# Kernel tuning notes

Measured on AMD Instinct MI355X. Metric: run time of the kernel, lower is better.

Reference implementation:

```python
import jax, jax.numpy as jnp
import numpy as np

B, T, D, U = 32, 1024, 2048, 1024

def setup_inputs() -> dict:
    key = jax.random.key(0)
    ks = jax.random.split(key, 8)
    s_d = 1.0 / np.sqrt(D)
    s_u = 1.0 / np.sqrt(U)
    return {
        "query": jax.random.normal(ks[0], (B, D), dtype=jnp.float32),
        "values": jax.random.normal(ks[1], (B, T, D), dtype=jnp.float32),
        "W1": jax.random.normal(ks[2], (D, U), dtype=jnp.float32) * s_d,
        "b1": jnp.zeros((U,), dtype=jnp.float32),
        "W2": jax.random.normal(ks[3], (D, U), dtype=jnp.float32) * s_d,
        "b2": jnp.zeros((U,), dtype=jnp.float32),
        "V": jax.random.normal(ks[4], (U, 1), dtype=jnp.float32) * s_u,
        "bv": jnp.zeros((1,), dtype=jnp.float32),
    }

def reference(query, values, W1, b1, W2, b2, V, bv):
    # keys: (B, T, U); query proj broadcast over time axis
    keys_proj = jnp.einsum('btd,du->btu', values, W1) + b1
    query_proj = (query @ W2 + b2)[:, None, :]          # (B, 1, U)
    score = jnp.tanh(keys_proj + query_proj) @ V + bv   # (B, T, 1)
    attention_weights = jax.nn.softmax(score, axis=1)   # (B, T, 1)
    context_vector = jnp.sum(attention_weights * values, axis=1)  # (B, D)
    return (context_vector, attention_weights)
```

## Files before the change

kernel.cpp:

```cpp
#include <hip/hip_runtime.h>
#include <math.h>

#define BB 32
#define TS 1024
#define DD 2048
#define UU 1024

typedef _Float16 f16x8 __attribute__((ext_vector_type(8)));
typedef _Float16 f16x2 __attribute__((ext_vector_type(2)));
typedef __fp16 fp16x2 __attribute__((ext_vector_type(2)));
typedef float f32x4 __attribute__((ext_vector_type(4)));

union H8 { f16x8 v; f16x2 p[4]; };

static __device__ inline f16x2 pk(float a, float b) {
  fp16x2 r = __builtin_amdgcn_cvt_pkrtz(a, b);
  return __builtin_bit_cast(f16x2, r);
}

static __device__ inline float fast_tanh(float x) {
  float e = __builtin_amdgcn_exp2f(x * 2.885390081777927f);
  return 1.f - 2.f * __builtin_amdgcn_rcpf(1.f + e);
}

static __device__ inline void gld16(const _Float16* g, _Float16* l) {
  __builtin_amdgcn_global_load_lds(
      (const __attribute__((address_space(1))) void*)g,
      (__attribute__((address_space(3))) void*)l, 16, 0, 0);
}

__global__ void zero_kernel(float* __restrict__ p) {
  p[blockIdx.x * 1024 + threadIdx.x] = 0.f;
}

__global__ __launch_bounds__(256) void qproj_kernel(
    const float* __restrict__ query, const float* __restrict__ W2,
    const float* __restrict__ b1, const float* __restrict__ b2,
    float* __restrict__ qpb) {
  __shared__ float qs[32][256];
  const int u0 = (blockIdx.x & 7) * 128;
  const int dsl = blockIdx.x >> 3;
  const int d0 = dsl * 256;
  const int tid = threadIdx.x;
  const int ul = tid & 127, half = tid >> 7;

  for (int i = tid; i < 32 * 64; i += 256) {
    int b = i >> 6, dq = i & 63;
    *(float4*)&qs[b][dq * 4] = *(const float4*)(query + b * DD + d0 + dq * 4);
  }
  __syncthreads();

  float acc[32];
#pragma unroll
  for (int b = 0; b < 32; ++b) acc[b] = 0.f;

  const float* wcol = W2 + (size_t)(d0 + half * 128) * UU + u0 + ul;
  for (int dd = 0; dd < 128; dd += 4) {
    float w0 = wcol[(size_t)(dd + 0) * UU];
    float w1 = wcol[(size_t)(dd + 1) * UU];
    float w2 = wcol[(size_t)(dd + 2) * UU];
    float w3 = wcol[(size_t)(dd + 3) * UU];
#pragma unroll
    for (int b = 0; b < 32; ++b) {
      float4 q4 = *(const float4*)&qs[b][half * 128 + dd];
      acc[b] += q4.x * w0 + q4.y * w1 + q4.z * w2 + q4.w * w3;
    }
  }

  const int u = u0 + ul;
  const float bias = (dsl == 0 && half == 0) ? (b1[u] + b2[u]) : 0.f;
#pragma unroll
  for (int b = 0; b < 32; ++b) atomicAdd(&qpb[b * UU + u], acc[b] + bias);
}

__global__ __launch_bounds__(256) void pack_values_kernel(
    const float* __restrict__ v, _Float16* __restrict__ vhp) {
  __shared__ _Float16 img[8192];
  const int mTile = blockIdx.x >> 5;
  const int kc = blockIdx.x & 31;
  const int tid = threadIdx.x;

#pragma unroll
  for (int i = 0; i < 4; ++i) {
    int idx = i * 256 + tid;
    int row = idx >> 3, khi = idx & 7;
    const float* src = v + ((size_t)(mTile * 128 + row)) * DD + kc * 64 + khi * 8;
    float4 x = *(const float4*)src;
    float4 y = *(const float4*)(src + 4);
    H8 h;
    h.p[0] = pk(x.x, x.y); h.p[1] = pk(x.z, x.w);
    h.p[2] = pk(y.x, y.y); h.p[3] = pk(y.z, y.w);
    *(f16x8*)&img[(khi * 128 + (row ^ khi)) * 8] = h.v;
  }
  __syncthreads();

  _Float16* out = vhp + ((size_t)mTile * 32 + kc) * 8192;
#pragma unroll
  for (int i = 0; i < 4; ++i) {
    int p = i * 256 + tid;
    int khi = p >> 7, row = p & 127;
    *(f16x8*)(out + (size_t)p * 8) = *(const f16x8*)&img[(khi * 128 + (row ^ khi)) * 8];
  }
}

__global__ __launch_bounds__(256) void pack_w1_kernel(
    const float* __restrict__ W1, _Float16* __restrict__ w1p) {
  __shared__ _Float16 img[8192];
  const int nTile = blockIdx.x >> 5;
  const int kc = blockIdx.x & 31;
  const int tid = threadIdx.x;

#pragma unroll
  for (int i = 0; i < 32; ++i) {
    int idx = i * 256 + tid;
    int ul = idx & 127, kl = idx >> 7;
    float x = W1[(size_t)(kc * 64 + kl) * UU + nTile * 128 + ul];
    int khi = kl >> 3, klo = kl & 7;
    img[(khi * 128 + (ul ^ khi)) * 8 + klo] = (_Float16)x;
  }
  __syncthreads();

  _Float16* out = w1p + ((size_t)nTile * 32 + kc) * 8192;
#pragma unroll
  for (int i = 0; i < 4; ++i) {
    int p = i * 256 + tid;
    int khi = p >> 7, row = p & 127;
    *(f16x8*)(out + (size_t)p * 8) = *(const f16x8*)&img[(khi * 128 + (row ^ khi)) * 8];
  }
}

__global__ __launch_bounds__(256) void score_gemm_p_kernel(
    const _Float16* __restrict__ vhp, const _Float16* __restrict__ w1p,
    const float* __restrict__ qpb, const float* __restrict__ V,
    float* __restrict__ score) {
  __shared__ _Float16 aS[8192];
  __shared__ _Float16 bS[8192];

  const int tid = threadIdx.x;
  const int r = blockIdx.x & 7, q = blockIdx.x >> 3;
  const int mTile = r * 32 + (q >> 3);
  const int nTile = q & 7;
  const int mBase = mTile * 128, nBase = nTile * 128;

  const int lane = tid & 63, wave = tid >> 6;
  const int wm = (wave & 1) * 64, wn = (wave >> 1) * 64;
  const int quad = lane >> 4, c16 = lane & 15;

  const _Float16* gA = vhp + (size_t)mTile * 32 * 8192 + lane * 8;
  const _Float16* gB = w1p + (size_t)nTile * 32 * 8192 + lane * 8;

  f32x4 acc[4][4];
#pragma unroll
  for (int mi = 0; mi < 4; ++mi)
#pragma unroll
    for (int ni = 0; ni < 4; ++ni) acc[mi][ni] = (f32x4)0.f;

  for (int kc = 0; kc < 32; ++kc) {
    __syncthreads();
#pragma unroll
    for (int j = 0; j < 4; ++j) {
      int s = wave * 4 + j;
      gld16(gA + (size_t)kc * 8192 + s * 512, &aS[s * 512]);
      gld16(gB + (size_t)kc * 8192 + s * 512, &bS[s * 512]);
    }
    __syncthreads();

#pragma unroll
    for (int h = 0; h < 2; ++h) {
      f16x8 af[4], bf[4];
#pragma unroll
      for (int i = 0; i < 4; ++i) {
        af[i] = *(const f16x8*)&aS[((h * 4 + quad) * 128 + wm + i * 16 + c16) * 8];
        bf[i] = *(const f16x8*)&bS[((h * 4 + quad) * 128 + wn + i * 16 + c16) * 8];
      }
#pragma unroll
      for (int mi = 0; mi < 4; ++mi)
#pragma unroll
        for (int ni = 0; ni < 4; ++ni)
          acc[mi][ni] = __builtin_amdgcn_mfma_f32_16x16x32_f16(
              af[mi], bf[ni], acc[mi][ni], 0, 0, 0);
    }
  }

  const int b = mBase >> 10;
  float qv[4], vv[4];
#pragma unroll
  for (int ni = 0; ni < 4; ++ni) {
    int ug = nBase + wn + ni * 16 + c16;
    qv[ni] = qpb[b * UU + ug];
    vv[ni] = V[ug];
  }
#pragma unroll
  for (int mi = 0; mi < 4; ++mi) {
#pragma unroll
    for (int reg = 0; reg < 4; ++reg) {
      float p = fast_tanh(acc[mi][0][reg] + qv[0]) * vv[0] +
                fast_tanh(acc[mi][1][reg] + qv[1]) * vv[1] +
                fast_tanh(acc[mi][2][reg] + qv[2]) * vv[2] +
                fast_tanh(acc[mi][3][reg] + qv[3]) * vv[3];
      p += __shfl_xor(p, 1, 64);
      p += __shfl_xor(p, 2, 64);
      p += __shfl_xor(p, 4, 64);
      p += __shfl_xor(p, 8, 64);
      if (c16 == 0) {
        int mrow = mBase + wm + mi * 16 + quad * 4 + reg;
        atomicAdd(&score[mrow], p);
      }
    }
  }
}

__global__ __launch_bounds__(256) void score_gemm_kernel(
    const float* __restrict__ values, const float* __restrict__ W1,
    const float* __restrict__ qpb, const float* __restrict__ V,
    float* __restrict__ score) {
  __shared__ _Float16 aS[4 * 128 * 8];
  __shared__ _Float16 bS[4 * 128 * 8];

  const int tid = threadIdx.x;
  const int mBase = (blockIdx.x >> 3) * 128;
  const int nBase = (blockIdx.x & 7) * 128;

  const int am = tid >> 1;
  const int akh = (tid & 1) * 16;
  const float* aG = values + (size_t)(mBase + am) * DD + akh;
  const int aOff0 = (((tid & 1) * 2) * 128 + am) * 8;
  const int bu2 = (tid & 63) * 2;
  const int bkq = tid >> 6;
  const float* bG = W1 + (size_t)(bkq * 8) * UU + nBase + bu2;
  const int bOff0 = (bkq * 128 + bu2) * 8;

  const int lane = tid & 63;
  const int wave = tid >> 6;
  const int wm = (wave & 1) * 64;
  const int wn = (wave >> 1) * 64;
  const int quad = lane >> 4;
  const int c16 = lane & 15;

  f32x4 acc[4][4];
#pragma unroll
  for (int mi = 0; mi < 4; ++mi)
#pragma unroll
    for (int ni = 0; ni < 4; ++ni) acc[mi][ni] = (f32x4)0.f;

  for (int k0 = 0; k0 < DD; k0 += 32) {
    float4 a0 = *(const float4*)(aG + k0 + 0);
    float4 a1 = *(const float4*)(aG + k0 + 4);
    float4 a2 = *(const float4*)(aG + k0 + 8);
    float4 a3 = *(const float4*)(aG + k0 + 12);
    const float* bRow = bG + (size_t)k0 * UU;
    float2 g0 = *(const float2*)(bRow + 0 * UU);
    float2 g1 = *(const float2*)(bRow + 1 * UU);
    float2 g2 = *(const float2*)(bRow + 2 * UU);
    float2 g3 = *(const float2*)(bRow + 3 * UU);
    float2 g4 = *(const float2*)(bRow + 4 * UU);
    float2 g5 = *(const float2*)(bRow + 5 * UU);
    float2 g6 = *(const float2*)(bRow + 6 * UU);
    float2 g7 = *(const float2*)(bRow + 7 * UU);

    __syncthreads();

    H8 ha0, ha1, hb0, hb1;
    ha0.p[0] = pk(a0.x, a0.y); ha0.p[1] = pk(a0.z, a0.w);
    ha0.p[2] = pk(a1.x, a1.y); ha0.p[3] = pk(a1.z, a1.w);
    ha1.p[0] = pk(a2.x, a2.y); ha1.p[1] = pk(a2.z, a2.w);
    ha1.p[2] = pk(a3.x, a3.y); ha1.p[3] = pk(a3.z, a3.w);
    *(f16x8*)&aS[aOff0] = ha0.v;
    *(f16x8*)&aS[aOff0 + 1024] = ha1.v;

    hb0.p[0] = pk(g0.x, g1.x); hb0.p[1] = pk(g2.x, g3.x);
    hb0.p[2] = pk(g4.x, g5.x); hb0.p[3] = pk(g6.x, g7.x);
    hb1.p[0] = pk(g0.y, g1.y); hb1.p[1] = pk(g2.y, g3.y);
    hb1.p[2] = pk(g4.y, g5.y); hb1.p[3] = pk(g6.y, g7.y);
    *(f16x8*)&bS[bOff0] = hb0.v;
    *(f16x8*)&bS[bOff0 + 8] = hb1.v;

    __syncthreads();

    f16x8 af[4], bf[4];
#pragma unroll
    for (int i = 0; i < 4; ++i) {
      af[i] = *(const f16x8*)&aS[(quad * 128 + wm + i * 16 + c16) * 8];
      bf[i] = *(const f16x8*)&bS[(quad * 128 + wn + i * 16 + c16) * 8];
    }
#pragma unroll
    for (int mi = 0; mi < 4; ++mi)
#pragma unroll
      for (int ni = 0; ni < 4; ++ni)
        acc[mi][ni] = __builtin_amdgcn_mfma_f32_16x16x32_f16(
            af[mi], bf[ni], acc[mi][ni], 0, 0, 0);
  }

  const int b = mBase >> 10;
  float qv[4], vv[4];
#pragma unroll
  for (int ni = 0; ni < 4; ++ni) {
    int ug = nBase + wn + ni * 16 + c16;
    qv[ni] = qpb[b * UU + ug];
    vv[ni] = V[ug];
  }
#pragma unroll
  for (int mi = 0; mi < 4; ++mi) {
#pragma unroll
    for (int reg = 0; reg < 4; ++reg) {
      float p = fast_tanh(acc[mi][0][reg] + qv[0]) * vv[0] +
                fast_tanh(acc[mi][1][reg] + qv[1]) * vv[1] +
                fast_tanh(acc[mi][2][reg] + qv[2]) * vv[2] +
                fast_tanh(acc[mi][3][reg] + qv[3]) * vv[3];
      p += __shfl_xor(p, 1, 64);
      p += __shfl_xor(p, 2, 64);
      p += __shfl_xor(p, 4, 64);
      p += __shfl_xor(p, 8, 64);
      if (c16 == 0) {
        int mrow = mBase + wm + mi * 16 + quad * 4 + reg;
        atomicAdd(&score[mrow], p);
      }
    }
  }
}

__global__ __launch_bounds__(256) void softmax_kernel(float* __restrict__ sw) {
  __shared__ float red[256];
  const int b = blockIdx.x;
  const int tid = threadIdx.x;
  float* s = sw + b * TS;

  float vals[4];
  float m = -1e30f;
#pragma unroll
  for (int i = 0; i < 4; ++i) {
    vals[i] = s[tid + 256 * i];
    m = fmaxf(m, vals[i]);
  }
  red[tid] = m;
  __syncthreads();
  for (int off = 128; off > 0; off >>= 1) {
    if (tid < off) red[tid] = fmaxf(red[tid], red[tid + off]);
    __syncthreads();
  }
  m = red[0];
  __syncthreads();

  float sum = 0.f;
#pragma unroll
  for (int i = 0; i < 4; ++i) {
    vals[i] = expf(vals[i] - m);
    sum += vals[i];
  }
  red[tid] = sum;
  __syncthreads();
  for (int off = 128; off > 0; off >>= 1) {
    if (tid < off) red[tid] += red[tid + off];
    __syncthreads();
  }
  const float inv = 1.f / red[0];
#pragma unroll
  for (int i = 0; i < 4; ++i) s[tid + 256 * i] = vals[i] * inv;
}

__global__ __launch_bounds__(256) void context_p_kernel(
    const _Float16* __restrict__ vhp, const float* __restrict__ weights,
    float* __restrict__ context) {
  __shared__ float wl[TS];
  const int b = blockIdx.x >> 5;
  const int kc = blockIdx.x & 31;
  const int tid = threadIdx.x;
  const int lane = tid & 63, wave = tid >> 6;

  for (int i = tid; i < TS; i += 256) wl[i] = weights[b * TS + i];
  __syncthreads();

  const int khiA = wave;
  const int khiB = wave + 4;

  float acc0[8], acc1[8];
#pragma unroll
  for (int j = 0; j < 8; ++j) { acc0[j] = 0.f; acc1[j] = 0.f; }

  for (int mt8 = 0; mt8 < 8; ++mt8) {
    const _Float16* base = vhp + ((size_t)(b * 8 + mt8) * 32 + kc) * 8192;
    const float* wrow = &wl[mt8 * 128];
#pragma unroll
    for (int half = 0; half < 2; ++half) {
      const int row = half * 64 + lane;
      const float wt = wrow[row];
      f16x8 vA = *(const f16x8*)&base[(khiA * 128 + row) * 8];
      f16x8 vB = *(const f16x8*)&base[(khiB * 128 + row) * 8];
#pragma unroll
      for (int j = 0; j < 8; ++j) {
        acc0[j] += wt * (float)vA[j];
        acc1[j] += wt * (float)vB[j];
      }
    }
  }

#pragma unroll
  for (int j = 0; j < 8; ++j) {
    float a = acc0[j], c = acc1[j];
#pragma unroll
    for (int off = 1; off < 64; off <<= 1) {
      a += __shfl_xor(a, off, 64);
      c += __shfl_xor(c, off, 64);
    }
    acc0[j] = a; acc1[j] = c;
  }

  if (lane == 0) {
    float* dst = context + b * DD + kc * 64;
#pragma unroll
    for (int j = 0; j < 8; ++j) {
      dst[khiA * 8 + j] = acc0[j];
      dst[khiB * 8 + j] = acc1[j];
    }
  }
}

__global__ __launch_bounds__(1024) void context_kernel(
    const float* __restrict__ values, const float* __restrict__ weights,
    float* __restrict__ context) {
  __shared__ float wl[TS];
  __shared__ float4 part[15][64];
  const int b = blockIdx.x >> 3;
  const int d0 = (blockIdx.x & 7) * 256;
  const int tid = threadIdx.x;
  const int slice = tid >> 6, dl = tid & 63;

  wl[tid] = weights[b * TS + tid];
  __syncthreads();

  const float* vb = values + ((size_t)b * TS + slice * 64) * DD + d0 + dl * 4;
  float4 acc = {0.f, 0.f, 0.f, 0.f};
#pragma unroll 8
  for (int t = 0; t < 64; ++t) {
    float w = wl[slice * 64 + t];
    float4 v4 = *(const float4*)(vb + (size_t)t * DD);
    acc.x += w * v4.x; acc.y += w * v4.y;
    acc.z += w * v4.z; acc.w += w * v4.w;
  }

  if (slice) part[slice - 1][dl] = acc;
  __syncthreads();
  if (slice == 0) {
#pragma unroll
    for (int i = 0; i < 15; ++i) {
      float4 p = part[i][dl];
      acc.x += p.x; acc.y += p.y; acc.z += p.z; acc.w += p.w;
    }
    *(float4*)(context + b * DD + d0 + dl * 4) = acc;
  }
}

extern "C" void kernel_launch(void* const* d_in, const int* in_sizes, int n_in,
                              void* d_out, int out_size, void* d_ws, size_t ws_size,
                              hipStream_t stream) {
  const float* query  = (const float*)d_in[0];
  const float* values = (const float*)d_in[1];
  const float* W1     = (const float*)d_in[2];
  const float* b1     = (const float*)d_in[3];
  const float* W2     = (const float*)d_in[4];
  const float* b2     = (const float*)d_in[5];
  const float* V      = (const float*)d_in[6];

  float* out = (float*)d_out;
  float* context = out;
  float* weights = out + BB * DD;

  float* qpb   = context;
  float* score = weights;

  const size_t need = (size_t)BB * TS * DD * 2 + (size_t)DD * UU * 2;
  const bool big_ws = ws_size >= need;

  zero_kernel<<<96, 1024, 0, stream>>>(out);
  qproj_kernel<<<64, 256, 0, stream>>>(query, W2, b1, b2, qpb);

  if (big_ws) {
    _Float16* vhp = (_Float16*)d_ws;
    _Float16* w1p = vhp + (size_t)BB * TS * DD;
    pack_values_kernel<<<256 * 32, 256, 0, stream>>>(values, vhp);
    pack_w1_kernel<<<8 * 32, 256, 0, stream>>>(W1, w1p);
    score_gemm_p_kernel<<<(BB * TS / 128) * (UU / 128), 256, 0, stream>>>(
        vhp, w1p, qpb, V, score);
    softmax_kernel<<<BB, 256, 0, stream>>>(score);
    context_p_kernel<<<BB * 32, 256, 0, stream>>>(vhp, weights, context);
  } else {
    score_gemm_kernel<<<(BB * TS / 128) * (UU / 128), 256, 0, stream>>>(
        values, W1, qpb, V, score);
    softmax_kernel<<<BB, 256, 0, stream>>>(score);
    context_kernel<<<BB * 8, 1024, 0, stream>>>(values, weights, context);
  }
}
```

Baseline: 627.1 us.

## Enlarge score GEMM tiles to 256x256 with double-buffered LDS pipeline

Replaces the 128x128 score GEMM with a 512-thread 256x256 tile kernel. It double-buffers LDS so the next K-slice loads while MFMAs run, raises wave priority during compute, and swizzles the block order. The aim is more operand reuse per global load and hiding load latency, paid for with more registers and LDS per block (128KB). It also doubles the qproj grid by halving its D-slice per block, and rewrites softmax to one element per thread using wave-shuffle reductions.

```diff
diff --git a/kernel.cpp b/kernel.cpp
--- a/kernel.cpp
+++ b/kernel.cpp
@@ -37,15 +37,15 @@
     const float* __restrict__ query, const float* __restrict__ W2,
     const float* __restrict__ b1, const float* __restrict__ b2,
     float* __restrict__ qpb) {
-  __shared__ float qs[32][256];
+  __shared__ float qs[32][128];
   const int u0 = (blockIdx.x & 7) * 128;
   const int dsl = blockIdx.x >> 3;
-  const int d0 = dsl * 256;
+  const int d0 = dsl * 128;
   const int tid = threadIdx.x;
   const int ul = tid & 127, half = tid >> 7;
 
-  for (int i = tid; i < 32 * 64; i += 256) {
-    int b = i >> 6, dq = i & 63;
+  for (int i = tid; i < 32 * 32; i += 256) {
+    int b = i >> 5, dq = i & 31;
     *(float4*)&qs[b][dq * 4] = *(const float4*)(query + b * DD + d0 + dq * 4);
   }
   __syncthreads();
@@ -54,15 +54,15 @@
 #pragma unroll
   for (int b = 0; b < 32; ++b) acc[b] = 0.f;
 
-  const float* wcol = W2 + (size_t)(d0 + half * 128) * UU + u0 + ul;
-  for (int dd = 0; dd < 128; dd += 4) {
+  const float* wcol = W2 + (size_t)(d0 + half * 64) * UU + u0 + ul;
+  for (int dd = 0; dd < 64; dd += 4) {
     float w0 = wcol[(size_t)(dd + 0) * UU];
     float w1 = wcol[(size_t)(dd + 1) * UU];
     float w2 = wcol[(size_t)(dd + 2) * UU];
     float w3 = wcol[(size_t)(dd + 3) * UU];
 #pragma unroll
     for (int b = 0; b < 32; ++b) {
-      float4 q4 = *(const float4*)&qs[b][half * 128 + dd];
+      float4 q4 = *(const float4*)&qs[b][half * 64 + dd];
       acc[b] += q4.x * w0 + q4.y * w1 + q4.z * w2 + q4.w * w3;
     }
   }
@@ -129,69 +129,101 @@
   }
 }
 
-__global__ __launch_bounds__(256) void score_gemm_p_kernel(
+__global__ __launch_bounds__(512, 2) void score_gemm_p2_kernel(
     const _Float16* __restrict__ vhp, const _Float16* __restrict__ w1p,
     const float* __restrict__ qpb, const float* __restrict__ V,
     float* __restrict__ score) {
-  __shared__ _Float16 aS[8192];
-  __shared__ _Float16 bS[8192];
-
-  const int tid = threadIdx.x;
-  const int r = blockIdx.x & 7, q = blockIdx.x >> 3;
-  const int mTile = r * 32 + (q >> 3);
-  const int nTile = q & 7;
-  const int mBase = mTile * 128, nBase = nTile * 128;
-
+  __shared__ _Float16 aS[2][16384];
+  __shared__ _Float16 bS[2][16384];
+
+  const int tid = threadIdx.x;
   const int lane = tid & 63, wave = tid >> 6;
-  const int wm = (wave & 1) * 64, wn = (wave >> 1) * 64;
+
+  const int swz = (blockIdx.x & 7) * 64 + (blockIdx.x >> 3);
+  const int mb = swz >> 2;
+  const int nb = swz & 3;
+
+  const int wr = wave >> 2;
+  const int wc = wave & 3;
   const int quad = lane >> 4, c16 = lane & 15;
 
-  const _Float16* gA = vhp + (size_t)mTile * 32 * 8192 + lane * 8;
-  const _Float16* gB = w1p + (size_t)nTile * 32 * 8192 + lane * 8;
-
-  f32x4 acc[4][4];
-#pragma unroll
-  for (int mi = 0; mi < 4; ++mi)
+  const _Float16* gA0 = vhp + ((size_t)(2 * mb + 0) * 32) * 8192 + lane * 8;
+  const _Float16* gA1 = vhp + ((size_t)(2 * mb + 1) * 32) * 8192 + lane * 8;
+  const _Float16* gB0 = w1p + ((size_t)(2 * nb + 0) * 32) * 8192 + lane * 8;
+  const _Float16* gB1 = w1p + ((size_t)(2 * nb + 1) * 32) * 8192 + lane * 8;
+
+  f32x4 acc[8][4];
+#pragma unroll
+  for (int mi = 0; mi < 8; ++mi)
 #pragma unroll
     for (int ni = 0; ni < 4; ++ni) acc[mi][ni] = (f32x4)0.f;
 
-  for (int kc = 0; kc < 32; ++kc) {
-    __syncthreads();
-#pragma unroll
-    for (int j = 0; j < 4; ++j) {
-      int s = wave * 4 + j;
-      gld16(gA + (size_t)kc * 8192 + s * 512, &aS[s * 512]);
-      gld16(gB + (size_t)kc * 8192 + s * 512, &bS[s * 512]);
-    }
-    __syncthreads();
-
-#pragma unroll
-    for (int h = 0; h < 2; ++h) {
-      f16x8 af[4], bf[4];
-#pragma unroll
-      for (int i = 0; i < 4; ++i) {
-        af[i] = *(const f16x8*)&aS[((h * 4 + quad) * 128 + wm + i * 16 + c16) * 8];
-        bf[i] = *(const f16x8*)&bS[((h * 4 + quad) * 128 + wn + i * 16 + c16) * 8];
-      }
-#pragma unroll
-      for (int mi = 0; mi < 4; ++mi)
-#pragma unroll
-        for (int ni = 0; ni < 4; ++ni)
-          acc[mi][ni] = __builtin_amdgcn_mfma_f32_16x16x32_f16(
-              af[mi], bf[ni], acc[mi][ni], 0, 0, 0);
-    }
-  }
-
-  const int b = mBase >> 10;
+  auto STAGE = [&](int kt, int sl) {
+#pragma unroll
+    for (int j = 0; j < 2; ++j) {
+      int s = wave * 2 + j;
+      gld16(gA0 + (size_t)kt * 8192 + s * 512, &aS[sl][0 * 8192 + s * 512]);
+      gld16(gA1 + (size_t)kt * 8192 + s * 512, &aS[sl][1 * 8192 + s * 512]);
+      gld16(gB0 + (size_t)kt * 8192 + s * 512, &bS[sl][0 * 8192 + s * 512]);
+      gld16(gB1 + (size_t)kt * 8192 + s * 512, &bS[sl][1 * 8192 + s * 512]);
+    }
+  };
+
+  STAGE(0, 0);
+
+  const int b = mb >> 2;
+  const int nBase = nb * 256;
   float qv[4], vv[4];
 #pragma unroll
   for (int ni = 0; ni < 4; ++ni) {
-    int ug = nBase + wn + ni * 16 + c16;
+    int ug = nBase + wc * 64 + ni * 16 + c16;
     qv[ni] = qpb[b * UU + ug];
     vv[ni] = V[ug];
   }
-#pragma unroll
-  for (int mi = 0; mi < 4; ++mi) {
+
+  __syncthreads();
+
+  const int aBase = wr * 8192 + c16 * 8;
+  const int bBase = (wc >> 1) * 8192 + ((wc & 1) * 64 + c16) * 8;
+
+  for (int it = 0; it < 32; ++it) {
+    const int cur = it & 1;
+
+    f16x8 bf[2][4];
+#pragma unroll
+    for (int hk = 0; hk < 2; ++hk)
+#pragma unroll
+      for (int ni = 0; ni < 4; ++ni)
+        bf[hk][ni] =
+            *(const f16x8*)&bS[cur][bBase + (((hk * 4 + quad) * 128) + ni * 16) * 8];
+
+    if (it + 1 < 32) STAGE(it + 1, cur ^ 1);
+
+    __builtin_amdgcn_s_setprio(1);
+#pragma unroll
+    for (int hk = 0; hk < 2; ++hk) {
+#pragma unroll
+      for (int mp = 0; mp < 4; ++mp) {
+        f16x8 a0 = *(const f16x8*)&aS[cur][aBase +
+            (((hk * 4 + quad) * 128) + (mp * 2 + 0) * 16) * 8];
+        f16x8 a1 = *(const f16x8*)&aS[cur][aBase +
+            (((hk * 4 + quad) * 128) + (mp * 2 + 1) * 16) * 8];
+#pragma unroll
+        for (int ni = 0; ni < 4; ++ni) {
+          acc[mp * 2 + 0][ni] = __builtin_amdgcn_mfma_f32_16x16x32_f16(
+              a0, bf[hk][ni], acc[mp * 2 + 0][ni], 0, 0, 0);
+          acc[mp * 2 + 1][ni] = __builtin_amdgcn_mfma_f32_16x16x32_f16(
+              a1, bf[hk][ni], acc[mp * 2 + 1][ni], 0, 0, 0);
+        }
+      }
+    }
+    __builtin_amdgcn_s_setprio(0);
+
+    __syncthreads();
+  }
+
+#pragma unroll
+  for (int mi = 0; mi < 8; ++mi) {
 #pragma unroll
     for (int reg = 0; reg < 4; ++reg) {
       float p = fast_tanh(acc[mi][0][reg] + qv[0]) * vv[0] +
@@ -203,7 +235,7 @@
       p += __shfl_xor(p, 4, 64);
       p += __shfl_xor(p, 8, 64);
       if (c16 == 0) {
-        int mrow = mBase + wm + mi * 16 + quad * 4 + reg;
+        int mrow = mb * 256 + wr * 128 + mi * 16 + quad * 4 + reg;
         atomicAdd(&score[mrow], p);
       }
     }
@@ -319,43 +351,36 @@
   }
 }
 
-__global__ __launch_bounds__(256) void softmax_kernel(float* __restrict__ sw) {
-  __shared__ float red[256];
+__global__ __launch_bounds__(1024) void softmax_kernel(float* __restrict__ sw) {
+  __shared__ float red[16];
   const int b = blockIdx.x;
   const int tid = threadIdx.x;
+  const int wid = tid >> 6, lane = tid & 63;
   float* s = sw + b * TS;
 
-  float vals[4];
-  float m = -1e30f;
-#pragma unroll
-  for (int i = 0; i < 4; ++i) {
-    vals[i] = s[tid + 256 * i];
-    m = fmaxf(m, vals[i]);
-  }
-  red[tid] = m;
-  __syncthreads();
-  for (int off = 128; off > 0; off >>= 1) {
-    if (tid < off) red[tid] = fmaxf(red[tid], red[tid + off]);
-    __syncthreads();
-  }
-  m = red[0];
-  __syncthreads();
-
-  float sum = 0.f;
-#pragma unroll
-  for (int i = 0; i < 4; ++i) {
-    vals[i] = expf(vals[i] - m);
-    sum += vals[i];
-  }
-  red[tid] = sum;
-  __syncthreads();
-  for (int off = 128; off > 0; off >>= 1) {
-    if (tid < off) red[tid] += red[tid + off];
-    __syncthreads();
-  }
-  const float inv = 1.f / red[0];
-#pragma unroll
-  for (int i = 0; i < 4; ++i) s[tid + 256 * i] = vals[i] * inv;
+  const float v = s[tid];
+
+  float m = v;
+#pragma unroll
+  for (int off = 32; off > 0; off >>= 1) m = fmaxf(m, __shfl_xor(m, off, 64));
+  if (lane == 0) red[wid] = m;
+  __syncthreads();
+  float mm = red[0];
+#pragma unroll
+  for (int i = 1; i < 16; ++i) mm = fmaxf(mm, red[i]);
+  __syncthreads();
+
+  const float e = expf(v - mm);
+  float sum = e;
+#pragma unroll
+  for (int off = 32; off > 0; off >>= 1) sum += __shfl_xor(sum, off, 64);
+  if (lane == 0) red[wid] = sum;
+  __syncthreads();
+  float tot = 0.f;
+#pragma unroll
+  for (int i = 0; i < 16; ++i) tot += red[i];
+
+  s[tid] = e * (1.f / tot);
 }
 
 __global__ __launch_bounds__(256) void context_p_kernel(
@@ -472,21 +497,21 @@
   const bool big_ws = ws_size >= need;
 
   zero_kernel<<<96, 1024, 0, stream>>>(out);
-  qproj_kernel<<<64, 256, 0, stream>>>(query, W2, b1, b2, qpb);
+  qproj_kernel<<<128, 256, 0, stream>>>(query, W2, b1, b2, qpb);
 
   if (big_ws) {
     _Float16* vhp = (_Float16*)d_ws;
     _Float16* w1p = vhp + (size_t)BB * TS * DD;
     pack_values_kernel<<<256 * 32, 256, 0, stream>>>(values, vhp);
     pack_w1_kernel<<<8 * 32, 256, 0, stream>>>(W1, w1p);
-    score_gemm_p_kernel<<<(BB * TS / 128) * (UU / 128), 256, 0, stream>>>(
+    score_gemm_p2_kernel<<<(BB * TS / 256) * (UU / 256), 512, 0, stream>>>(
         vhp, w1p, qpb, V, score);
-    softmax_kernel<<<BB, 256, 0, stream>>>(score);
+    softmax_kernel<<<BB, 1024, 0, stream>>>(score);
     context_p_kernel<<<BB * 32, 256, 0, stream>>>(vhp, weights, context);
   } else {
     score_gemm_kernel<<<(BB * TS / 128) * (UU / 128), 256, 0, stream>>>(
         values, W1, qpb, V, score);
-    softmax_kernel<<<BB, 256, 0, stream>>>(score);
+    softmax_kernel<<<BB, 1024, 0, stream>>>(score);
     context_kernel<<<BB * 8, 1024, 0, stream>>>(values, weights, context);
   }
 }
```

After: 594.4 us. 5.2% less time.
